# Optimization experiments

Measured on AMD Instinct MI355X. Metric: run time of the kernel, lower is better.

## Reference

```python
import jax, jax.numpy as jnp
import numpy as np

B, N = 256, 64          # molecules, atoms per molecule
EMB = 64                # atom embedding dim
G = 64                  # n_gaussians
HID = 128               # interaction hidden
OUT = 512               # output_dim
GAUSS_WIDTH = 0.5


def setup_inputs() -> dict:
    key = jax.random.key(0)
    ks = jax.random.split(key, 10)
    atomic_nums = jax.random.randint(ks[0], (B, N), 0, 120, dtype=jnp.int64 if jax.config.x64_enabled else jnp.int32)
    coords = jax.random.normal(ks[1], (B, N, 3), dtype=jnp.float32) * 3.0
    embed_table = jax.random.normal(ks[2], (120, EMB), dtype=jnp.float32)
    # interaction: Linear(128->128), GELU, Linear(128->128); weights stored (in, out)
    W1 = jax.random.normal(ks[3], (EMB + G, HID), dtype=jnp.float32) / np.sqrt(EMB + G)
    b1 = jnp.zeros((HID,), dtype=jnp.float32)
    W2 = jax.random.normal(ks[4], (HID, HID), dtype=jnp.float32) / np.sqrt(HID)
    b2 = jnp.zeros((HID,), dtype=jnp.float32)
    # output_proj: Linear(128 -> 512)
    Wo = jax.random.normal(ks[5], (HID, OUT), dtype=jnp.float32) / np.sqrt(HID)
    bo = jnp.zeros((OUT,), dtype=jnp.float32)
    centers = jnp.linspace(0.0, 10.0, G).astype(jnp.float32)
    return {"atomic_nums": atomic_nums, "coords": coords, "embed_table": embed_table,
            "W1": W1, "b1": b1, "W2": W2, "b2": b2, "Wo": Wo, "bo": bo, "centers": centers}


def reference(atomic_nums, coords, embed_table, W1, b1, W2, b2, Wo, bo, centers):
    # per-atom embedding: [B,N,EMB]
    emb = embed_table[atomic_nums]
    # pairwise distances: [B,N,N]; guard sqrt(0) for diagonal
    diff = coords[:, :, None, :] - coords[:, None, :, :]
    sq = jnp.sum(diff * diff, axis=-1)
    pos = sq > 0
    dists = jnp.where(pos, jnp.sqrt(jnp.where(pos, sq, 1.0)), 0.0)
    # Gaussian smearing: [B,N,N,G]
    gauss = jnp.exp(-0.5 * jnp.square((dists[..., None] - centers) / GAUSS_WIDTH))
    # mean over neighbor axis j: [B,N,G]
    avg_gauss = gauss.mean(axis=2)
    feat = jnp.concatenate([emb, avg_gauss], axis=-1)  # [B,N,EMB+G]
    h = jax.nn.gelu(feat @ W1 + b1, approximate=False) @ W2 + b2  # [B,N,HID]
    mol = h.mean(axis=1)  # [B,HID]
    return mol @ Wo + bo  # [B,OUT]
```

## Files before the change

kernel.cpp:

```cpp
#include <hip/hip_runtime.h>
#include <math.h>

namespace {
constexpr int NB   = 256;
constexpr int NA   = 64;
constexpr int EMBD = 64;
constexpr int HIDD = 128;
constexpr int OUTD = 512;
constexpr int FPS  = 136;
constexpr int DSTR = 68;

typedef __attribute__((ext_vector_type(8))) short bfrag8;
typedef __attribute__((ext_vector_type(4))) float floatx4;

__device__ __forceinline__ unsigned short bf16_rne(float f) {
    unsigned u = __float_as_uint(f);
    u += 0x7fffu + ((u >> 16) & 1u);
    return (unsigned short)(u >> 16);
}

__device__ __forceinline__ float gelu_fast(float x) {
    const float ax = fabsf(x) * 0.7071067811865475f;
    const float t  = __builtin_amdgcn_rcpf(fmaf(0.3275911f, ax, 1.0f));
    float p = fmaf(1.061405429f, t, -1.453152027f);
    p = fmaf(p, t, 1.421413741f);
    p = fmaf(p, t, -0.284496736f);
    p = fmaf(p, t, 0.254829592f);
    p = p * t;
    const float e = __builtin_amdgcn_exp2f(-1.4426950408889634f * ax * ax);
    const float erfx = copysignf(fmaf(-p, e, 1.0f), x);
    const float hx   = 0.5f * x;
    return fmaf(hx, erfx, hx);
}

__global__ __launch_bounds__(512, 4)
void mlip_front(const int*   __restrict__ atomic_nums,
                const float* __restrict__ coords,
                const float* __restrict__ embed_table,
                const float* __restrict__ W1, const float* __restrict__ b1,
                const float* __restrict__ W2,
                const float* __restrict__ centers,
                float*       __restrict__ ws)
{
    const int bid  = blockIdx.x;
    const int mol  = bid >> 1, h = bid & 1;
    const int tid  = threadIdx.x;
    const int lane = tid & 63;
    const int wid  = tid >> 6;

    __shared__ float s_dist[32 * DSTR];
    __shared__ short s_w[16384];
    __shared__ short s_fhi[32][FPS];
    __shared__ float s_molS[HIDD];

    const int wn      = wid >> 1;
    const int lrow    = lane & 15, g4 = lane >> 4;
    const int arow    = ((wid & 1) << 4) + lrow;
    const int colbase = (wn << 5) + lrow;

    const int gcol = tid & 127, kc = tid >> 7;

    const int grow = tid >> 4;
    const int gch  = (tid >> 2) & 3;
    const int jq   = tid & 3;

    const float b1a = b1[colbase];
    const float b1b = b1[colbase + 16];
    const float c0  = centers[gch << 4];

    if (tid < HIDD) s_molS[tid] = 0.0f;

    float w1v[16];
#pragma unroll
    for (int a = 0; a < 2; ++a) {
        const int slot = (a << 9) + tid;
        const int fg = slot >> 6, ls = slot & 63;
        const int k0 = ((fg >> 3) << 5) + ((ls >> 4) << 3);
        const int n  = ((fg & 7) << 4) + (ls & 15);
        const float* src = W1 + (size_t)k0 * HIDD + n;
#pragma unroll
        for (int r = 0; r < 8; ++r) w1v[a * 8 + r] = src[(size_t)r * HIDD];
    }

    const float* cbase = coords + (size_t)mol * NA * 3;
    const float cx = cbase[lane * 3 + 0];
    const float cy = cbase[lane * 3 + 1];
    const float cz = cbase[lane * 3 + 2];

    {
        const int i = tid >> 4, e4 = (tid & 15) << 2;
        const int z = atomic_nums[mol * NA + (h << 5) + i];
        const float4 ev = *(const float4*)(embed_table + (size_t)z * EMBD + e4);
        short4 h4;
        const float v[4] = {ev.x, ev.y, ev.z, ev.w};
        short* hp = (short*)&h4;
#pragma unroll
        for (int q = 0; q < 4; ++q) hp[q] = (short)bf16_rne(v[q]);
        *(short4*)&s_fhi[i][e4] = h4;
    }

#pragma unroll
    for (int it = 0; it < 4; ++it) {
        const int i  = (wid << 2) + it;
        const int gi = (h << 5) + i;
        const float xi = __shfl(cx, gi, 64);
        const float yi = __shfl(cy, gi, 64);
        const float zi = __shfl(cz, gi, 64);
        const float dx = xi - cx, dy = yi - cy, dz = zi - cz;
        const float sq = dx * dx + dy * dy + dz * dz;
        s_dist[i * DSTR + lane] = sq > 0.0f ? sqrtf(sq) : 0.0f;
    }

#pragma unroll
    for (int a = 0; a < 2; ++a) {
        unsigned Hu[4];
#pragma unroll
        for (int p = 0; p < 4; ++p) {
            const float x = w1v[a * 8 + 2 * p], y = w1v[a * 8 + 2 * p + 1];
            unsigned hh;
            asm("v_cvt_pk_bf16_f32 %0, %1, %2" : "=v"(hh) : "v"(x), "v"(y));
            Hu[p] = hh;
        }
        const int slot = (a << 9) + tid;
        const int base = ((slot >> 6) << 9) + (slot & 63) * 8;
        *(uint4*)&s_w[base] = make_uint4(Hu[0], Hu[1], Hu[2], Hu[3]);
    }

#pragma unroll
    for (int a = 0; a < 2; ++a) {
        const int slot = ((a + 2) << 9) + tid;
        const int fg = slot >> 6, ls = slot & 63;
        const int k0 = ((fg >> 3) << 5) + ((ls >> 4) << 3);
        const int n  = ((fg & 7) << 4) + (ls & 15);
        const float* src = W1 + (size_t)k0 * HIDD + n;
#pragma unroll
        for (int r = 0; r < 8; ++r) w1v[a * 8 + r] = src[(size_t)r * HIDD];
    }

    {
        constexpr float L2E   = 1.4426950408889634f;
        constexpr float DELTA = 10.0f / 63.0f;
        constexpr float K2L   = -2.0f * L2E;
        constexpr float UA    = 4.0f * DELTA * L2E;
        const float P1  = 0.95085835f,  P2  = 0.81745274f, P3  = 0.63539088f,
                    P4  = 0.44653019f,  P5  = 0.28372112f, P6  = 0.16299117f,
                    P7  = 0.08465801f,  P8  = 0.03975530f, P9  = 0.01688004f,
                    P10 = 0.00647989f,  P11 = 0.00224901f, P12 = 0.00070576f,
                    P13 = 0.00020024f,  P14 = 5.136543e-5f, P15 = 1.191313e-5f;

        float acc[16];
#pragma unroll
        for (int q = 0; q < 16; ++q) acc[q] = 0.0f;

        const float* drow = &s_dist[grow * DSTR + (jq << 4)];
#pragma unroll
        for (int j4 = 0; j4 < 4; ++j4) {
            const float4 d4 = *(const float4*)(drow + (j4 << 2));
            const float dv[4] = {d4.x, d4.y, d4.z, d4.w};
#pragma unroll
            for (int jj = 0; jj < 4; ++jj) {
                const float x  = dv[jj] - c0;
                const float A  = __builtin_amdgcn_exp2f(K2L * x * x);
                const float r  = __builtin_amdgcn_exp2f(UA * x);
                const float r2 = r * r, r4 = r2 * r2;
                float s0 = A, s1 = A * r, s2 = A * r2, s3 = s1 * r2;
                acc[0] += s0;
                acc[1]  = fmaf(s1, P1,  acc[1]);
                acc[2]  = fmaf(s2, P2,  acc[2]);
                acc[3]  = fmaf(s3, P3,  acc[3]);
                s0 *= r4; s1 *= r4; s2 *= r4; s3 *= r4;
                acc[4]  = fmaf(s0, P4,  acc[4]);
                acc[5]  = fmaf(s1, P5,  acc[5]);
                acc[6]  = fmaf(s2, P6,  acc[6]);
                acc[7]  = fmaf(s3, P7,  acc[7]);
                s0 *= r4; s1 *= r4; s2 *= r4; s3 *= r4;
                acc[8]  = fmaf(s0, P8,  acc[8]);
                acc[9]  = fmaf(s1, P9,  acc[9]);
                acc[10] = fmaf(s2, P10, acc[10]);
                acc[11] = fmaf(s3, P11, acc[11]);
                s0 *= r4; s1 *= r4; s2 *= r4; s3 *= r4;
                acc[12] = fmaf(s0, P12, acc[12]);
                acc[13] = fmaf(s1, P13, acc[13]);
                acc[14] = fmaf(s2, P14, acc[14]);
                acc[15] = fmaf(s3, P15, acc[15]);
            }
        }
#pragma unroll
        for (int q = 0; q < 16; ++q) {
            acc[q] += __shfl_xor(acc[q], 1, 64);
            acc[q] += __shfl_xor(acc[q], 2, 64);
        }
        if (jq == 0) {
            unsigned* hp = (unsigned*)&s_fhi[grow][EMBD + (gch << 4)];
#pragma unroll
            for (int q2 = 0; q2 < 8; ++q2) {
                const unsigned h0 = bf16_rne(acc[2 * q2]     * (1.0f / 64.0f));
                const unsigned h1 = bf16_rne(acc[2 * q2 + 1] * (1.0f / 64.0f));
                hp[q2] = h0 | (h1 << 16);
            }
        }
    }

#pragma unroll
    for (int a = 0; a < 2; ++a) {
        unsigned Hu[4];
#pragma unroll
        for (int p = 0; p < 4; ++p) {
            const float x = w1v[a * 8 + 2 * p], y = w1v[a * 8 + 2 * p + 1];
            unsigned hh;
            asm("v_cvt_pk_bf16_f32 %0, %1, %2" : "=v"(hh) : "v"(x), "v"(y));
            Hu[p] = hh;
        }
        const int slot = ((a + 2) << 9) + tid;
        const int base = ((slot >> 6) << 9) + (slot & 63) * 8;
        *(uint4*)&s_w[base] = make_uint4(Hu[0], Hu[1], Hu[2], Hu[3]);
    }
    __syncthreads();

    float w2ra[16];
    {
        floatx4 acc0 = {0,0,0,0}, acc1 = {0,0,0,0};
#pragma unroll
        for (int ks = 0; ks < 4; ++ks) {
            const int k0 = (ks << 5) + (g4 << 3);
            const bfrag8 ahi = *(const bfrag8*)&s_fhi[arow][k0];
#pragma unroll
            for (int nt = 0; nt < 2; ++nt) {
                const int base = ((((ks << 3) + (wn << 1) + nt) << 6) + lane) << 3;
                const bfrag8 bhi = *(const bfrag8*)&s_w[base];
                if (nt) acc1 = __builtin_amdgcn_mfma_f32_16x16x32_bf16(ahi, bhi, acc1, 0, 0, 0);
                else    acc0 = __builtin_amdgcn_mfma_f32_16x16x32_bf16(ahi, bhi, acc0, 0, 0, 0);
            }
        }

        {
            const float* src = W2 + (size_t)(kc << 5) * HIDD + gcol;
#pragma unroll
            for (int q = 0; q < 16; ++q) w2ra[q] = src[(size_t)q * HIDD];
        }

#pragma unroll
        for (int nt = 0; nt < 2; ++nt) {
            const float bb = nt ? b1b : b1a;
            const floatx4 a = nt ? acc1 : acc0;
            float s = gelu_fast(a[0] + bb) + gelu_fast(a[1] + bb)
                    + gelu_fast(a[2] + bb) + gelu_fast(a[3] + bb);
            s += __shfl_xor(s, 16, 64);
            s += __shfl_xor(s, 32, 64);
            if (lane < 16) atomicAdd(&s_molS[colbase + (nt << 4)], s);
        }
    }
    __syncthreads();

    {
        float w2rb[16];
        const float* src2 = W2 + (size_t)((kc << 5) + 16) * HIDD + gcol;
#pragma unroll
        for (int q = 0; q < 16; ++q) w2rb[q] = src2[(size_t)q * HIDD];

        float acc = 0.0f;
        float4 m4[4];
#pragma unroll
        for (int p = 0; p < 4; ++p) m4[p] = *(const float4*)&s_molS[(kc << 5) + (p << 2)];
        const float* ms = (const float*)m4;
#pragma unroll
        for (int q = 0; q < 16; ++q) acc = fmaf(ms[q], w2ra[q], acc);
        float4 m4b[4];
#pragma unroll
        for (int p = 0; p < 4; ++p) m4b[p] = *(const float4*)&s_molS[(kc << 5) + 16 + (p << 2)];
        const float* ms2 = (const float*)m4b;
#pragma unroll
        for (int q = 0; q < 16; ++q) acc = fmaf(ms2[q], w2rb[q], acc);

        s_dist[(kc << 7) + gcol] = acc;
    }
    __syncthreads();

    if (tid < HIDD) {
        const float u = ((s_dist[tid] + s_dist[128 + tid])
                       + (s_dist[256 + tid] + s_dist[384 + tid])) * (1.0f / 64.0f);
        ws[(size_t)mol * 256 + (h << 7) + tid] = u;
    }
}

__global__ __launch_bounds__(512, 2)
void mlip_tail(const float* __restrict__ b2,
               const float* __restrict__ Wo, const float* __restrict__ bo,
               const float* __restrict__ ws, float* __restrict__ out)
{
    const int mol = blockIdx.x;
    const int tid = threadIdx.x;
    __shared__ float s_molv[HIDD];

    if (tid < HIDD)
        s_molv[tid] = (ws[(size_t)mol * 256 + tid] + ws[(size_t)mol * 256 + 128 + tid])
                      + b2[tid];
    __syncthreads();

    float a0 = 0.f, a1 = 0.f, a2 = 0.f, a3 = 0.f;
    const float* wop = Wo + tid;
#pragma unroll 8
    for (int k = 0; k < HIDD; k += 4) {
        a0 = fmaf(s_molv[k + 0], wop[(size_t)(k + 0) << 9], a0);
        a1 = fmaf(s_molv[k + 1], wop[(size_t)(k + 1) << 9], a1);
        a2 = fmaf(s_molv[k + 2], wop[(size_t)(k + 2) << 9], a2);
        a3 = fmaf(s_molv[k + 3], wop[(size_t)(k + 3) << 9], a3);
    }
    out[(size_t)mol * OUTD + tid] = ((a0 + a1) + (a2 + a3)) + bo[tid];
}
}

extern "C" void kernel_launch(void* const* d_in, const int* in_sizes, int n_in,
                              void* d_out, int out_size, void* d_ws, size_t ws_size,
                              hipStream_t stream) {
    const int*   atomic_nums = (const int*)  d_in[0];
    const float* coords      = (const float*)d_in[1];
    const float* embed_table = (const float*)d_in[2];
    const float* W1          = (const float*)d_in[3];
    const float* b1          = (const float*)d_in[4];
    const float* W2          = (const float*)d_in[5];
    const float* b2          = (const float*)d_in[6];
    const float* Wo          = (const float*)d_in[7];
    const float* bo          = (const float*)d_in[8];
    const float* centers     = (const float*)d_in[9];
    float*       out         = (float*)d_out;
    float*       wsf         = (float*)d_ws;

    mlip_front<<<2 * NB, 512, 0, stream>>>(atomic_nums, coords, embed_table,
                                           W1, b1, W2, centers, wsf);
    mlip_tail<<<NB, 512, 0, stream>>>(b2, Wo, bo, wsf, out);
}
```

Measured before the change: 19.28 us.

## Split each molecule across four front blocks of sixteen atoms

Each front block now handles 16 atoms instead of 32, so the grid grows from 512 to 1024 blocks. Each wave computes one 16-column MFMA tile, the Gaussian reduction spreads across 8 lanes per row, and the atomic adds into shared memory become plain stores. The tail kernel now sums four partial vectors per molecule. The intent is more parallelism and occupancy (launch bounds raised to 6 blocks). The cost is that each block still loads all of W1 and W2, so weight-load overhead per atom doubles.

```diff
diff --git a/kernel.cpp b/kernel.cpp
--- a/kernel.cpp
+++ b/kernel.cpp
@@ -33,7 +33,7 @@
     return fmaf(hx, erfx, hx);
 }
 
-__global__ __launch_bounds__(512, 4)
+__global__ __launch_bounds__(512, 6)
 void mlip_front(const int*   __restrict__ atomic_nums,
                 const float* __restrict__ coords,
                 const float* __restrict__ embed_table,
@@ -43,32 +43,27 @@
                 float*       __restrict__ ws)
 {
     const int bid  = blockIdx.x;
-    const int mol  = bid >> 1, h = bid & 1;
+    const int mol  = bid >> 2, qh = bid & 3;
     const int tid  = threadIdx.x;
     const int lane = tid & 63;
     const int wid  = tid >> 6;
 
-    __shared__ float s_dist[32 * DSTR];
+    __shared__ float s_dist[16 * DSTR];
     __shared__ short s_w[16384];
-    __shared__ short s_fhi[32][FPS];
+    __shared__ short s_fhi[16][FPS];
     __shared__ float s_molS[HIDD];
 
-    const int wn      = wid >> 1;
     const int lrow    = lane & 15, g4 = lane >> 4;
-    const int arow    = ((wid & 1) << 4) + lrow;
-    const int colbase = (wn << 5) + lrow;
+    const int colbase = (wid << 4) + lrow;
 
     const int gcol = tid & 127, kc = tid >> 7;
 
-    const int grow = tid >> 4;
-    const int gch  = (tid >> 2) & 3;
-    const int jq   = tid & 3;
-
-    const float b1a = b1[colbase];
-    const float b1b = b1[colbase + 16];
+    const int grow = tid >> 5;
+    const int gch  = (tid >> 3) & 3;
+    const int jq   = tid & 7;
+
+    const float b1r = b1[colbase];
     const float c0  = centers[gch << 4];
-
-    if (tid < HIDD) s_molS[tid] = 0.0f;
 
     float w1v[16];
 #pragma unroll
@@ -88,21 +83,17 @@
     const float cz = cbase[lane * 3 + 2];
 
     {
-        const int i = tid >> 4, e4 = (tid & 15) << 2;
-        const int z = atomic_nums[mol * NA + (h << 5) + i];
-        const float4 ev = *(const float4*)(embed_table + (size_t)z * EMBD + e4);
-        short4 h4;
-        const float v[4] = {ev.x, ev.y, ev.z, ev.w};
-        short* hp = (short*)&h4;
-#pragma unroll
-        for (int q = 0; q < 4; ++q) hp[q] = (short)bf16_rne(v[q]);
-        *(short4*)&s_fhi[i][e4] = h4;
-    }
-
-#pragma unroll
-    for (int it = 0; it < 4; ++it) {
-        const int i  = (wid << 2) + it;
-        const int gi = (h << 5) + i;
+        const int i = tid >> 5, c2 = (tid & 31) << 1;
+        const int z = atomic_nums[mol * NA + (qh << 4) + i];
+        const float2 ev = *(const float2*)(embed_table + (size_t)z * EMBD + c2);
+        const unsigned h0 = bf16_rne(ev.x), h1 = bf16_rne(ev.y);
+        *(unsigned*)&s_fhi[i][c2] = h0 | (h1 << 16);
+    }
+
+#pragma unroll
+    for (int it = 0; it < 2; ++it) {
+        const int i  = (wid << 1) + it;
+        const int gi = (qh << 4) + i;
         const float xi = __shfl(cx, gi, 64);
         const float yi = __shfl(cy, gi, 64);
         const float zi = __shfl(cz, gi, 64);
@@ -152,9 +143,9 @@
 #pragma unroll
         for (int q = 0; q < 16; ++q) acc[q] = 0.0f;
 
-        const float* drow = &s_dist[grow * DSTR + (jq << 4)];
-#pragma unroll
-        for (int j4 = 0; j4 < 4; ++j4) {
+        const float* drow = &s_dist[grow * DSTR + (jq << 3)];
+#pragma unroll
+        for (int j4 = 0; j4 < 2; ++j4) {
             const float4 d4 = *(const float4*)(drow + (j4 << 2));
             const float dv[4] = {d4.x, d4.y, d4.z, d4.w};
 #pragma unroll
@@ -189,6 +180,7 @@
         for (int q = 0; q < 16; ++q) {
             acc[q] += __shfl_xor(acc[q], 1, 64);
             acc[q] += __shfl_xor(acc[q], 2, 64);
+            acc[q] += __shfl_xor(acc[q], 4, 64);
         }
         if (jq == 0) {
             unsigned* hp = (unsigned*)&s_fhi[grow][EMBD + (gch << 4)];
@@ -219,18 +211,14 @@
 
     float w2ra[16];
     {
-        floatx4 acc0 = {0,0,0,0}, acc1 = {0,0,0,0};
+        floatx4 acc0 = {0,0,0,0};
 #pragma unroll
         for (int ks = 0; ks < 4; ++ks) {
             const int k0 = (ks << 5) + (g4 << 3);
-            const bfrag8 ahi = *(const bfrag8*)&s_fhi[arow][k0];
-#pragma unroll
-            for (int nt = 0; nt < 2; ++nt) {
-                const int base = ((((ks << 3) + (wn << 1) + nt) << 6) + lane) << 3;
-                const bfrag8 bhi = *(const bfrag8*)&s_w[base];
-                if (nt) acc1 = __builtin_amdgcn_mfma_f32_16x16x32_bf16(ahi, bhi, acc1, 0, 0, 0);
-                else    acc0 = __builtin_amdgcn_mfma_f32_16x16x32_bf16(ahi, bhi, acc0, 0, 0, 0);
-            }
+            const bfrag8 ahi = *(const bfrag8*)&s_fhi[lrow][k0];
+            const int base = ((((ks << 3) + wid) << 6) + lane) << 3;
+            const bfrag8 bhi = *(const bfrag8*)&s_w[base];
+            acc0 = __builtin_amdgcn_mfma_f32_16x16x32_bf16(ahi, bhi, acc0, 0, 0, 0);
         }
 
         {
@@ -239,16 +227,11 @@
             for (int q = 0; q < 16; ++q) w2ra[q] = src[(size_t)q * HIDD];
         }
 
-#pragma unroll
-        for (int nt = 0; nt < 2; ++nt) {
-            const float bb = nt ? b1b : b1a;
-            const floatx4 a = nt ? acc1 : acc0;
-            float s = gelu_fast(a[0] + bb) + gelu_fast(a[1] + bb)
-                    + gelu_fast(a[2] + bb) + gelu_fast(a[3] + bb);
-            s += __shfl_xor(s, 16, 64);
-            s += __shfl_xor(s, 32, 64);
-            if (lane < 16) atomicAdd(&s_molS[colbase + (nt << 4)], s);
-        }
+        float s = gelu_fast(acc0[0] + b1r) + gelu_fast(acc0[1] + b1r)
+                + gelu_fast(acc0[2] + b1r) + gelu_fast(acc0[3] + b1r);
+        s += __shfl_xor(s, 16, 64);
+        s += __shfl_xor(s, 32, 64);
+        if (lane < 16) s_molS[colbase] = s;
     }
     __syncthreads();
 
@@ -279,7 +262,7 @@
     if (tid < HIDD) {
         const float u = ((s_dist[tid] + s_dist[128 + tid])
                        + (s_dist[256 + tid] + s_dist[384 + tid])) * (1.0f / 64.0f);
-        ws[(size_t)mol * 256 + (h << 7) + tid] = u;
+        ws[(size_t)mol * 512 + (qh << 7) + tid] = u;
     }
 }
 
@@ -292,9 +275,11 @@
     const int tid = threadIdx.x;
     __shared__ float s_molv[HIDD];
 
-    if (tid < HIDD)
-        s_molv[tid] = (ws[(size_t)mol * 256 + tid] + ws[(size_t)mol * 256 + 128 + tid])
+    if (tid < HIDD) {
+        const float* u = ws + (size_t)mol * 512;
+        s_molv[tid] = ((u[tid] + u[128 + tid]) + (u[256 + tid] + u[384 + tid]))
                       + b2[tid];
+    }
     __syncthreads();
 
     float a0 = 0.f, a1 = 0.f, a2 = 0.f, a3 = 0.f;
@@ -326,7 +311,7 @@
     float*       out         = (float*)d_out;
     float*       wsf         = (float*)d_ws;
 
-    mlip_front<<<2 * NB, 512, 0, stream>>>(atomic_nums, coords, embed_table,
+    mlip_front<<<4 * NB, 512, 0, stream>>>(atomic_nums, coords, embed_table,
                                            W1, b1, W2, centers, wsf);
     mlip_tail<<<NB, 512, 0, stream>>>(b2, Wo, bo, wsf, out);
 }
```

New measurement: 22.16 us. 1.15x slower.
